# Optimization experiments

Hardware: AMD Instinct MI355X
Metric: run time of the kernel (lower is better)

## Reference

```python
import jax, jax.numpy as jnp
import numpy as np

B, N, D, H, L = 4, 256, 512, 8, 3
HD = D // H
K_SPARSE = max(1, int(N * 0.1))  # top-k edges per node
EPS = 1e-5  # torch LayerNorm default


def _mha(x, Wqkv, bqkv, Wo, bo):
    b, n, d = x.shape
    qkv = x @ Wqkv + bqkv
    q, k, v = jnp.split(qkv, 3, axis=-1)
    rs = lambda t: t.reshape(b, n, H, HD).transpose(0, 2, 1, 3)
    q, k, v = rs(q), rs(k), rs(v)
    att = jax.nn.softmax(jnp.einsum('bhqd,bhkd->bhqk', q, k) * (HD ** -0.5), axis=-1)
    out = jnp.einsum('bhqk,bhkd->bhqd', att, v).transpose(0, 2, 1, 3).reshape(b, n, d)
    return out @ Wo + bo


def _ln(x, g, b):
    m = x.mean(-1, keepdims=True)
    v = ((x - m) ** 2).mean(-1, keepdims=True)
    return (x - m) / jnp.sqrt(v + EPS) * g + b


def setup_inputs() -> dict:
    key = jax.random.key(0)
    ks = iter(jax.random.split(key, 32))
    rn = lambda *s: jax.random.normal(next(ks), s, jnp.float32) * 0.02
    return {
        'x': jax.random.normal(next(ks), (B, N, D), jnp.float32),
        'adjacency': jax.random.uniform(next(ks), (B, N, N), jnp.float32),
        'Wqkv': rn(L, D, 3 * D), 'bqkv': rn(L, 3 * D),
        'Wo': rn(L, D, D), 'bo': rn(L, D),
        'Wp1': rn(L - 1, D, D // 2), 'bp1': rn(L - 1, D // 2),
        'Wp2': rn(L - 1, D // 2, D), 'bp2': rn(L - 1, D),
        'Wfuse': rn(L * D, D), 'bfuse': rn(D),
        'ln_g': jnp.ones((D,), jnp.float32), 'ln_b': jnp.zeros((D,), jnp.float32),
        'We1': rn(2 * D, D), 'be1': rn(D), 'We2': rn(D, 1), 'be2': rn(1),
        'Ws_qkv': rn(D, 3 * D), 'bs_qkv': rn(3 * D),
        'Ws_o': rn(D, D), 'bs_o': rn(D),
    }


def reference(x, adjacency, Wqkv, bqkv, Wo, bo, Wp1, bp1, Wp2, bp2, Wfuse, bfuse,
              ln_g, ln_b, We1, be1, We2, be2, Ws_qkv, bs_qkv, Ws_o, bs_o):
    # --- HierarchicalGraphAttention ---
    cur = x
    level_outs = []
    for l in range(L):  # fixed small hierarchy loop
        a = _mha(cur, Wqkv[l], bqkv[l], Wo[l], bo[l])
        level_outs.append(a)
        if l < L - 1:
            p = jax.nn.relu(a @ Wp1[l] + bp1[l]) @ Wp2[l] + bp2[l]
            cur = p.reshape(B, -1, 2, D).mean(axis=2)  # pairwise pooling halves nodes
    # upsample each level back to N nodes (repeat_interleave), fuse
    fused = [jnp.repeat(o, N // o.shape[1], axis=1) for o in level_outs]
    hier = _ln(jax.nn.relu(jnp.concatenate(fused, axis=-1) @ Wfuse + bfuse), ln_g, ln_b)

    # --- SparseGraphOperations: O(N^2) edge scoring + per-row top-k ---
    # cat([x_i, x_j]) @ We1 == x_i @ We1[:D] + x_j @ We1[D:]
    hi = hier @ We1[:D]                      # [B,N,D]
    hj = hier @ We1[D:] + be1                # [B,N,D]
    pre = hi[:, :, None, :] + hj[:, None, :, :]  # [B,N,N,D]
    scores = jax.nn.sigmoid((jax.nn.relu(pre) @ We2 + be2)[..., 0])  # [B,N,N]
    scores = jnp.where(jnp.eye(N, dtype=bool)[None], 0.0, scores)    # i != j only
    _, idx = jax.lax.top_k(scores, K_SPARSE)  # [B,N,K]
    sparse_adj = jnp.zeros((B, N, N), jnp.float32).at[
        jnp.arange(B)[:, None, None], jnp.arange(N)[None, :, None], idx].set(1.0)

    attended = _mha(hier, Ws_qkv, bs_qkv, Ws_o, bs_o)
    return attended, sparse_adj
```

## Files before the change

### kernel.cpp

```cpp
#include <hip/hip_runtime.h>
#include <math.h>


template <int TM>
__global__ __launch_bounds__(256) void gemm_v6(
    const float* __restrict__ A, const float* __restrict__ W,
    const float* __restrict__ bias, float* __restrict__ C,
    int M, int N, int K, int flags, int wmode,
    const float* __restrict__ W2, const float* __restrict__ bias2)
{
    constexpr int RT = TM / 16;
    __shared__ float As[16][TM + 4];
    __shared__ float Ws[16][68];

    const int tid = threadIdx.x;
    const int tx = tid & 15, ty = tid >> 4;
    const int bm = blockIdx.y * TM, bn = blockIdx.x * 64;

    const float* Wp = W;
    const float* bp = bias;
    int wn = N, wcol = bn;
    if (wmode == 1) {
        int seg = (bm >= 1536) ? 2 : (bm >= 1024) ? 1 : 0;
        Wp += (size_t)seg * 262144;
    } else if (wmode == 3) {
        if (bn < 1536)      { wn = 1536; wcol = bn; }
        else if (bn < 2048) { Wp = W2;           wn = 512; wcol = bn - 1536; bp = nullptr; }
        else                { Wp = W2 + 262144;  wn = 512; wcol = bn - 2048; bp = bias2; }
    }

    constexpr int AV = (TM == 64) ? 4 : 2;
    const int ar = (TM == 64) ? (tid >> 2) : (tid >> 3);
    const int ac = (TM == 64) ? ((tid & 3) << 2) : ((tid & 7) << 1);
    const int wr = tid >> 4;
    const int wc = (tid & 15) << 2;

    const float* Aptr = A + (size_t)(bm + ar) * K + ac;
    const float* Wptr = Wp + (size_t)wr * wn + wcol + wc;

    float acc[RT][4] = {};
    float ra[AV], rw[4];

#define LOADREGS(k0_) do {                                                   \
        const float* ap_ = Aptr + (k0_);                                     \
        if constexpr (TM == 64) {                                            \
            float4 v_ = *(const float4*)ap_;                                 \
            ra[0]=v_.x; ra[1]=v_.y; ra[2]=v_.z; ra[3]=v_.w;                  \
        } else {                                                             \
            float2 v_ = *(const float2*)ap_; ra[0]=v_.x; ra[1]=v_.y;         \
        }                                                                    \
        float4 w_ = *(const float4*)(Wptr + (size_t)(k0_) * wn);             \
        rw[0]=w_.x; rw[1]=w_.y; rw[2]=w_.z; rw[3]=w_.w; } while (0)

    LOADREGS(0);

    for (int k0 = 0; k0 < K; k0 += 16) {
        if (k0) __syncthreads();
        #pragma unroll
        for (int u = 0; u < AV; ++u) As[ac + u][ar] = ra[u];
        #pragma unroll
        for (int u = 0; u < 4; ++u) Ws[wr][wc + u] = rw[u];
        __syncthreads();

        if (k0 + 16 < K) LOADREGS(k0 + 16);

        #pragma unroll
        for (int kk = 0; kk < 16; ++kk) {
            float a[RT];
            if constexpr (RT == 4) {
                float4 t = *(const float4*)&As[kk][ty * 4];
                a[0]=t.x; a[1]=t.y; a[2]=t.z; a[3]=t.w;
            } else {
                float2 t = *(const float2*)&As[kk][ty * 2];
                a[0]=t.x; a[1]=t.y;
            }
            float4 tw = *(const float4*)&Ws[kk][tx * 4];
            float w[4] = {tw.x, tw.y, tw.z, tw.w};
            #pragma unroll
            for (int i = 0; i < RT; ++i)
                #pragma unroll
                for (int j = 0; j < 4; ++j)
                    acc[i][j] = fmaf(a[i], w[j], acc[i][j]);
        }
    }
#undef LOADREGS

    #pragma unroll
    for (int j = 0; j < 4; ++j) {
        const int cn = bn + tx * 4 + j;
        const float bv = bp ? bp[wcol + tx * 4 + j] : 0.f;
        if (flags & 2) {
            #pragma unroll
            for (int pi = 0; pi < RT / 2; ++pi) {
                float f0 = acc[2 * pi][j] + bv;
                float f1 = acc[2 * pi + 1][j] + bv;
                if (flags & 1) { f0 = fmaxf(f0, 0.f); f1 = fmaxf(f1, 0.f); }
                int prow = ((bm + ty * RT) >> 1) + pi;
                C[(size_t)prow * N + cn] = (f0 + f1) * 0.5f;
            }
        } else {
            #pragma unroll
            for (int i = 0; i < RT; ++i) {
                float f = acc[i][j] + bv;
                if (flags & 1) f = fmaxf(f, 0.f);
                C[(size_t)(bm + ty * RT + i) * N + cn] = f;
            }
        }
    }
}

template <int NT>
__global__ __launch_bounds__(256) void attn_v3(
    const float* __restrict__ qkv, float* __restrict__ out, int n, int qstride)
{
    const int lane = threadIdx.x & 63;
    const int w    = threadIdx.x >> 6;
    const int h = blockIdx.y, b = blockIdx.z;
    const int q0 = blockIdx.x * 16;
    const size_t base = (size_t)b * n * qstride;

    __shared__ float q_lds[16][64];
    __shared__ float kv_lds[64][68];
    __shared__ float p_lds[16][256];

    {
        int r = threadIdx.x >> 4, c4 = (threadIdx.x & 15) << 2;
        float4 v = *(const float4*)(qkv + base + (size_t)(q0 + r) * qstride + h * 64 + c4);
        q_lds[r][c4 + 0] = v.x; q_lds[r][c4 + 1] = v.y;
        q_lds[r][c4 + 2] = v.z; q_lds[r][c4 + 3] = v.w;
    }

    const int r0 = w * 4;
    const int sr = threadIdx.x >> 2;
    const int sq = threadIdx.x & 3;

    float s[4][NT];

    #pragma unroll
    for (int t = 0; t < NT; ++t) {
        const int j0 = t * 64;
        __syncthreads();
        {
            const float* src = qkv + base + (size_t)(j0 + sr) * qstride + 512 + h * 64;
            #pragma unroll
            for (int u = 0; u < 4; ++u) {
                int c = u * 4 + sq;
                float4 v = *(const float4*)(src + c * 4);
                *(float4*)&kv_lds[sr][c * 4] = v;
            }
        }
        __syncthreads();
        float c0 = 0.f, c1 = 0.f, c2 = 0.f, c3 = 0.f;
        #pragma unroll
        for (int d = 0; d < 64; d += 4) {
            const float4 kv = *(const float4*)&kv_lds[lane][d];
            const float4 qa = *(const float4*)&q_lds[r0 + 0][d];
            const float4 qb = *(const float4*)&q_lds[r0 + 1][d];
            const float4 qc = *(const float4*)&q_lds[r0 + 2][d];
            const float4 qd = *(const float4*)&q_lds[r0 + 3][d];
            c0 = fmaf(qa.x, kv.x, c0); c0 = fmaf(qa.y, kv.y, c0);
            c0 = fmaf(qa.z, kv.z, c0); c0 = fmaf(qa.w, kv.w, c0);
            c1 = fmaf(qb.x, kv.x, c1); c1 = fmaf(qb.y, kv.y, c1);
            c1 = fmaf(qb.z, kv.z, c1); c1 = fmaf(qb.w, kv.w, c1);
            c2 = fmaf(qc.x, kv.x, c2); c2 = fmaf(qc.y, kv.y, c2);
            c2 = fmaf(qc.z, kv.z, c2); c2 = fmaf(qc.w, kv.w, c2);
            c3 = fmaf(qd.x, kv.x, c3); c3 = fmaf(qd.y, kv.y, c3);
            c3 = fmaf(qd.z, kv.z, c3); c3 = fmaf(qd.w, kv.w, c3);
        }
        s[0][t] = c0 * 0.125f; s[1][t] = c1 * 0.125f;
        s[2][t] = c2 * 0.125f; s[3][t] = c3 * 0.125f;
    }

    double inv[4];
    #pragma unroll
    for (int qr = 0; qr < 4; ++qr) {
        float m = s[qr][0];
        #pragma unroll
        for (int t = 1; t < NT; ++t) m = fmaxf(m, s[qr][t]);
        #pragma unroll
        for (int off = 32; off; off >>= 1) m = fmaxf(m, __shfl_xor(m, off));
        double sum = 0.0;
        #pragma unroll
        for (int t = 0; t < NT; ++t) {
            float p = expf(s[qr][t] - m);
            p_lds[r0 + qr][t * 64 + lane] = p;
            sum += (double)p;
        }
        #pragma unroll
        for (int off = 32; off; off >>= 1) sum += __shfl_xor(sum, off);
        inv[qr] = 1.0 / sum;
    }

    float o0 = 0.f, o1 = 0.f, o2 = 0.f, o3 = 0.f;
    #pragma unroll
    for (int t = 0; t < NT; ++t) {
        const int j0 = t * 64;
        __syncthreads();
        {
            const float* src = qkv + base + (size_t)(j0 + sr) * qstride + 1024 + h * 64;
            #pragma unroll
            for (int u = 0; u < 4; ++u) {
                int c = u * 4 + sq;
                float4 v = *(const float4*)(src + c * 4);
                kv_lds[c * 4 + 0][sr] = v.x;
                kv_lds[c * 4 + 1][sr] = v.y;
                kv_lds[c * 4 + 2][sr] = v.z;
                kv_lds[c * 4 + 3][sr] = v.w;
            }
        }
        __syncthreads();
        #pragma unroll
        for (int jl = 0; jl < 64; jl += 4) {
            const float4 vv = *(const float4*)&kv_lds[lane][jl];
            const float4 pa = *(const float4*)&p_lds[r0 + 0][t * 64 + jl];
            const float4 pb = *(const float4*)&p_lds[r0 + 1][t * 64 + jl];
            const float4 pc = *(const float4*)&p_lds[r0 + 2][t * 64 + jl];
            const float4 pd = *(const float4*)&p_lds[r0 + 3][t * 64 + jl];
            o0 = fmaf(pa.x, vv.x, o0); o0 = fmaf(pa.y, vv.y, o0);
            o0 = fmaf(pa.z, vv.z, o0); o0 = fmaf(pa.w, vv.w, o0);
            o1 = fmaf(pb.x, vv.x, o1); o1 = fmaf(pb.y, vv.y, o1);
            o1 = fmaf(pb.z, vv.z, o1); o1 = fmaf(pb.w, vv.w, o1);
            o2 = fmaf(pc.x, vv.x, o2); o2 = fmaf(pc.y, vv.y, o2);
            o2 = fmaf(pc.z, vv.z, o2); o2 = fmaf(pc.w, vv.w, o2);
            o3 = fmaf(pd.x, vv.x, o3); o3 = fmaf(pd.y, vv.y, o3);
            o3 = fmaf(pd.z, vv.z, o3); o3 = fmaf(pd.w, vv.w, o3);
        }
    }
    const size_t obase = ((size_t)(b * n + q0 + r0)) * 512 + h * 64 + lane;
    out[obase + 0 * 512] = (float)((double)o0 * inv[0]);
    out[obase + 1 * 512] = (float)((double)o1 * inv[1]);
    out[obase + 2 * 512] = (float)((double)o2 * inv[2]);
    out[obase + 3 * 512] = (float)((double)o3 * inv[3]);
}

__global__ __launch_bounds__(64) void ln3_kernel(
    const float* __restrict__ y, const float* __restrict__ bf,
    const float* __restrict__ g, const float* __restrict__ bta,
    float* __restrict__ out)
{
    const int r = blockIdx.x, lane = threadIdx.x;
    const int b = r >> 8, i = r & 255;
    const float* y0 = y + (size_t)r * 512;
    const float* y1 = y + (size_t)(1024 + b * 128 + (i >> 1)) * 512;
    const float* y2 = y + (size_t)(1536 + b * 64 + (i >> 2)) * 512;
    double v[8];
    double sum = 0.0;
    #pragma unroll
    for (int t = 0; t < 8; ++t) {
        int d = t * 64 + lane;
        double s = (double)y0[d] + (double)y1[d] + (double)y2[d] + (double)bf[d];
        s = s > 0.0 ? s : 0.0;
        v[t] = s; sum += s;
    }
    #pragma unroll
    for (int off = 32; off; off >>= 1) sum += __shfl_xor(sum, off);
    const double mean = sum * (1.0 / 512.0);
    double ss = 0.0;
    #pragma unroll
    for (int t = 0; t < 8; ++t) { double d = v[t] - mean; ss += d * d; }
    #pragma unroll
    for (int off = 32; off; off >>= 1) ss += __shfl_xor(ss, off);
    const double rstd = 1.0 / sqrt(ss * (1.0 / 512.0) + 1e-5);
    #pragma unroll
    for (int t = 0; t < 8; ++t) {
        int d = t * 64 + lane;
        out[(size_t)r * 512 + d] =
            (float)((v[t] - mean) * rstd * (double)g[d] + (double)bta[d]);
    }
}

__global__ __launch_bounds__(256) void scores_v4(
    const float* __restrict__ hq, int stride, int off,
    const float* __restrict__ We2, const float* __restrict__ be2,
    float* __restrict__ S)
{
    __shared__ float Hi[128][34];
    __shared__ float Hj[128][34];
    const int b = blockIdx.z;
    const int i0 = blockIdx.y * 32, j0 = blockIdx.x * 32;
    const int tid = threadIdx.x;
    const int tx = tid & 15, ty = tid >> 4;

    const int si = tid >> 3;
    const int sd = (tid & 7) << 2;

    const float* hip = hq + (size_t)(b * 256 + i0 + si) * stride + off + sd;
    const float* hjp = hq + (size_t)(b * 256 + j0 + si) * stride + off + 512 + sd;

    double a00 = 0.0, a01 = 0.0, a10 = 0.0, a11 = 0.0;

    for (int k0 = 0; k0 < 512; k0 += 128) {
        __syncthreads();
        #pragma unroll
        for (int u = 0; u < 4; ++u) {
            const int dch = u * 32 + sd;
            float4 v = *(const float4*)(hip + k0 + u * 32);
            Hi[dch + 0][si] = v.x; Hi[dch + 1][si] = v.y;
            Hi[dch + 2][si] = v.z; Hi[dch + 3][si] = v.w;
            float4 w = *(const float4*)(hjp + k0 + u * 32);
            Hj[dch + 0][si] = w.x; Hj[dch + 1][si] = w.y;
            Hj[dch + 2][si] = w.z; Hj[dch + 3][si] = w.w;
        }
        __syncthreads();
        #pragma unroll 16
        for (int kk = 0; kk < 128; ++kk) {
            const double wv = (double)We2[k0 + kk];
            const float2 hi = *(const float2*)&Hi[kk][ty * 2];
            const float2 hj = *(const float2*)&Hj[kk][tx * 2];
            a00 += (double)fmaxf(hi.x + hj.x, 0.f) * wv;
            a01 += (double)fmaxf(hi.x + hj.y, 0.f) * wv;
            a10 += (double)fmaxf(hi.y + hj.x, 0.f) * wv;
            a11 += (double)fmaxf(hi.y + hj.y, 0.f) * wv;
        }
    }

    const double bb = (double)be2[0];
    const int gi0 = i0 + ty * 2, gj0 = j0 + tx * 2;
    double zz[2][2] = {{a00, a01}, {a10, a11}};
    #pragma unroll
    for (int ii = 0; ii < 2; ++ii)
        #pragma unroll
        for (int jj = 0; jj < 2; ++jj) {
            double z = zz[ii][jj] + bb;
            float sc_ = (float)(1.0 / (1.0 + exp(-z)));
            if (gi0 + ii == gj0 + jj) sc_ = 0.f;
            S[(size_t)(b * 256 + gi0 + ii) * 256 + gj0 + jj] = sc_;
        }
}

__global__ __launch_bounds__(64) void topk_kernel(
    const float* __restrict__ S, float* __restrict__ out)
{
    const int row = blockIdx.x;
    const int lane = threadIdx.x;
    float v[4]; int sel[4] = {0, 0, 0, 0};
    #pragma unroll
    for (int t = 0; t < 4; ++t) v[t] = S[(size_t)row * 256 + t * 64 + lane];
    for (int it = 0; it < 25; ++it) {
        float bv = v[0]; int bi = lane;
        #pragma unroll
        for (int t = 1; t < 4; ++t) {
            int idx = t * 64 + lane;
            if (v[t] > bv) { bv = v[t]; bi = idx; }
        }
        #pragma unroll
        for (int off = 32; off; off >>= 1) {
            float ov = __shfl_xor(bv, off);
            int   oi = __shfl_xor(bi, off);
            if (ov > bv || (ov == bv && oi < bi)) { bv = ov; bi = oi; }
        }
        if ((bi & 63) == lane) { int t = bi >> 6; sel[t] = 1; v[t] = -INFINITY; }
    }
    #pragma unroll
    for (int t = 0; t < 4; ++t)
        out[(size_t)row * 256 + t * 64 + lane] = (float)sel[t];
}

extern "C" void kernel_launch(void* const* d_in, const int* in_sizes, int n_in,
                              void* d_out, int out_size, void* d_ws, size_t ws_size,
                              hipStream_t stream)
{
    const float* x      = (const float*)d_in[0];
    const float* Wqkv   = (const float*)d_in[2];
    const float* bqkv   = (const float*)d_in[3];
    const float* Wo     = (const float*)d_in[4];
    const float* bo     = (const float*)d_in[5];
    const float* Wp1    = (const float*)d_in[6];
    const float* bp1    = (const float*)d_in[7];
    const float* Wp2    = (const float*)d_in[8];
    const float* bp2    = (const float*)d_in[9];
    const float* Wfuse  = (const float*)d_in[10];
    const float* bfuse  = (const float*)d_in[11];
    const float* ln_g   = (const float*)d_in[12];
    const float* ln_b   = (const float*)d_in[13];
    const float* We1    = (const float*)d_in[14];
    const float* be1    = (const float*)d_in[15];
    const float* We2    = (const float*)d_in[16];
    const float* be2    = (const float*)d_in[17];
    const float* Ws_qkv = (const float*)d_in[18];
    const float* bs_qkv = (const float*)d_in[19];
    const float* Ws_o   = (const float*)d_in[20];
    const float* bs_o   = (const float*)d_in[21];

    float* out_att    = (float*)d_out;
    float* out_sparse = out_att + 4 * 256 * 512;

    float* ws    = (float*)d_ws;
    float* qkvb  = ws;
    float* attnb = qkvb + 1572864;
    float* lvls  = attnb + 524288;
    float* poolb = lvls + 917504;
    float* curb  = poolb + 131072;
    float* hier  = curb + 262144;
    float* scb   = hier + 524288;
    float* qh    = scb + 262144;

    float* lvl0 = lvls;
    float* lvl1 = lvls + 1024 * 512;
    float* lvl2 = lvls + 1536 * 512;

    auto G64 = [&](const float* A, const float* W, const float* bias, float* C,
                   int M, int N, int K, int flags, int wmode,
                   const float* W2 = nullptr, const float* bias2 = nullptr) {
        gemm_v6<64><<<dim3(N / 64, M / 64), 256, 0, stream>>>(
            A, W, bias, C, M, N, K, flags, wmode, W2, bias2);
    };
    auto G32 = [&](const float* A, const float* W, const float* bias, float* C,
                   int M, int N, int K, int flags, int wmode) {
        gemm_v6<32><<<dim3(N / 64, M / 32), 256, 0, stream>>>(
            A, W, bias, C, M, N, K, flags, wmode, nullptr, nullptr);
    };

    G64(x, Wqkv, bqkv, qkvb, 1024, 1536, 512, 0, 0);
    attn_v3<4><<<dim3(16, 8, 4), 256, 0, stream>>>(qkvb, attnb, 256, 1536);
    G32(attnb, Wo, bo, lvl0, 1024, 512, 512, 0, 0);
    G32(lvl0, Wp1, bp1, poolb, 1024, 256, 512, 3, 0);
    G32(poolb, Wp2, bp2, curb, 512, 512, 256, 0, 0);

    G64(curb, Wqkv + 512 * 1536, bqkv + 1536, qkvb, 512, 1536, 512, 0, 0);
    attn_v3<2><<<dim3(8, 8, 4), 256, 0, stream>>>(qkvb, attnb, 128, 1536);
    G32(attnb, Wo + 512 * 512, bo + 512, lvl1, 512, 512, 512, 0, 0);
    G32(lvl1, Wp1 + 512 * 256, bp1 + 256, poolb, 512, 256, 512, 3, 0);
    G32(poolb, Wp2 + 256 * 512, bp2 + 512, curb, 256, 512, 256, 0, 0);

    G32(curb, Wqkv + 2 * 512 * 1536, bqkv + 2 * 1536, qkvb, 256, 1536, 512, 0, 0);
    attn_v3<1><<<dim3(4, 8, 4), 256, 0, stream>>>(qkvb, attnb, 64, 1536);
    G32(attnb, Wo + 2 * 512 * 512, bo + 2 * 512, lvl2, 256, 512, 512, 0, 0);

    G64(lvls, Wfuse, nullptr, qkvb, 1792, 512, 512, 0, 1);
    ln3_kernel<<<1024, 64, 0, stream>>>(qkvb, bfuse, ln_g, ln_b, hier);

    G64(hier, Ws_qkv, bs_qkv, qh, 1024, 2560, 512, 0, 3, We1, be1);

    scores_v4<<<dim3(8, 8, 4), 256, 0, stream>>>(qh, 2560, 1536, We2, be2, scb);
    topk_kernel<<<1024, 64, 0, stream>>>(scb, out_sparse);

    attn_v3<4><<<dim3(16, 8, 4), 256, 0, stream>>>(qh, attnb, 256, 2560);
    G32(attnb, Ws_o, bs_o, out_att, 1024, 512, 512, 0, 0);
}
```

Baseline: 391.4 us.

## Use bf16 MFMA GEMMs for final attention projections with transposed weight conversion

Adds a bf16 MFMA GEMM kernel and a weight transpose-and-convert kernel, and runs the final self-attention QKV and output projections on matrix cores. The layernorm and attention kernels also emit bf16 copies of their outputs to feed these GEMMs. The fused QKV+We1 GEMM is split so the edge-score projection stays in fp32 on the old path. This trades extra conversion kernels, extra writes and reduced precision for faster matrix-core math on the final-stage GEMMs.

Result: no change. 383.9 us (-1.9%).

```diff
diff --git a/kernel.cpp b/kernel.cpp
--- a/kernel.cpp
+++ b/kernel.cpp
@@ -1,13 +1,22 @@
 #include <hip/hip_runtime.h>
 #include <math.h>
 
+
+typedef __attribute__((ext_vector_type(8))) short bf16x8;
+typedef __attribute__((ext_vector_type(4))) float f32x4;
+typedef __attribute__((ext_vector_type(8))) unsigned short ushort8v;
+
+__device__ __forceinline__ unsigned short f2bf(float x) {
+    union { float f; unsigned int u; } c; c.f = x;
+    unsigned int r = (c.u + 0x7fffu + ((c.u >> 16) & 1u)) >> 16;
+    return (unsigned short)r;
+}
 
 template <int TM>
 __global__ __launch_bounds__(256) void gemm_v6(
     const float* __restrict__ A, const float* __restrict__ W,
     const float* __restrict__ bias, float* __restrict__ C,
-    int M, int N, int K, int flags, int wmode,
-    const float* __restrict__ W2, const float* __restrict__ bias2)
+    int M, int N, int K, int flags, int wmode)
 {
     constexpr int RT = TM / 16;
     __shared__ float As[16][TM + 4];
@@ -23,10 +32,9 @@
     if (wmode == 1) {
         int seg = (bm >= 1536) ? 2 : (bm >= 1024) ? 1 : 0;
         Wp += (size_t)seg * 262144;
-    } else if (wmode == 3) {
-        if (bn < 1536)      { wn = 1536; wcol = bn; }
-        else if (bn < 2048) { Wp = W2;           wn = 512; wcol = bn - 1536; bp = nullptr; }
-        else                { Wp = W2 + 262144;  wn = 512; wcol = bn - 2048; bp = bias2; }
+    } else if (wmode == 2) {
+        if (bn >= 512) Wp += 262144; else bp = nullptr;
+        wn = 512; wcol = bn & 511;
     }
 
     constexpr int AV = (TM == 64) ? 4 : 2;
@@ -109,9 +117,81 @@
     }
 }
 
+__global__ __launch_bounds__(256) void cvtT_kernel(
+    const float* __restrict__ W, unsigned short* __restrict__ Wt, int K, int N)
+{
+    __shared__ unsigned short t[64][72];
+    const int n0 = blockIdx.x * 64, k0 = blockIdx.y * 64;
+    const int tid = threadIdx.x;
+    const int rr = tid >> 4, c4 = (tid & 15) << 2;
+    #pragma unroll
+    for (int u = 0; u < 4; ++u) {
+        const float4 v = *(const float4*)(W + (size_t)(k0 + rr + u * 16) * N + n0 + c4);
+        t[c4 + 0][rr + u * 16] = f2bf(v.x);
+        t[c4 + 1][rr + u * 16] = f2bf(v.y);
+        t[c4 + 2][rr + u * 16] = f2bf(v.z);
+        t[c4 + 3][rr + u * 16] = f2bf(v.w);
+    }
+    __syncthreads();
+    const int orow = tid >> 2, oc = (tid & 3) << 4;
+    unsigned short* dst = Wt + (size_t)(n0 + orow) * K + k0 + oc;
+    *(ushort8v*)(dst + 0) = *(const ushort8v*)&t[orow][oc + 0];
+    *(ushort8v*)(dst + 8) = *(const ushort8v*)&t[orow][oc + 8];
+}
+
+__global__ __launch_bounds__(256) void mfma_gemm(
+    const unsigned short* __restrict__ Ab, const unsigned short* __restrict__ Bt,
+    const float* __restrict__ bias, float* __restrict__ C,
+    int M, int N, int K, int ldc)
+{
+    const int lane = threadIdx.x & 63;
+    const int wv = threadIdx.x >> 6;
+    const int bn = blockIdx.x * 64;
+    const int bm = blockIdx.y * 128 + wv * 32;
+    const int l15 = lane & 15;
+    const int kb = (lane >> 4) * 8;
+
+    const unsigned short* a0p = Ab + (size_t)(bm + l15) * K + kb;
+    const unsigned short* a1p = a0p + (size_t)16 * K;
+    const unsigned short* bp0 = Bt + (size_t)(bn + l15) * K + kb;
+
+    f32x4 acc[2][4];
+    #pragma unroll
+    for (int i = 0; i < 2; ++i)
+        #pragma unroll
+        for (int j = 0; j < 4; ++j)
+            acc[i][j] = (f32x4){0.f, 0.f, 0.f, 0.f};
+
+    for (int k0 = 0; k0 < K; k0 += 32) {
+        const bf16x8 a0 = *(const bf16x8*)(a0p + k0);
+        const bf16x8 a1 = *(const bf16x8*)(a1p + k0);
+        #pragma unroll
+        for (int nf = 0; nf < 4; ++nf) {
+            const bf16x8 b = *(const bf16x8*)(bp0 + (size_t)nf * 16 * K + k0);
+            acc[0][nf] = __builtin_amdgcn_mfma_f32_16x16x32_bf16(a0, b, acc[0][nf], 0, 0, 0);
+            acc[1][nf] = __builtin_amdgcn_mfma_f32_16x16x32_bf16(a1, b, acc[1][nf], 0, 0, 0);
+        }
+    }
+
+    const int r0 = (lane >> 4) * 4;
+    #pragma unroll
+    for (int mf = 0; mf < 2; ++mf)
+        #pragma unroll
+        for (int nf = 0; nf < 4; ++nf) {
+            const int col = bn + nf * 16 + l15;
+            const float bv = bias ? bias[col] : 0.f;
+            #pragma unroll
+            for (int r = 0; r < 4; ++r) {
+                const int row = bm + mf * 16 + r0 + r;
+                C[(size_t)row * ldc + col] = acc[mf][nf][r] + bv;
+            }
+        }
+}
+
 template <int NT>
 __global__ __launch_bounds__(256) void attn_v3(
-    const float* __restrict__ qkv, float* __restrict__ out, int n, int qstride)
+    const float* __restrict__ qkv, float* __restrict__ out,
+    unsigned short* __restrict__ outb, int n, int qstride)
 {
     const int lane = threadIdx.x & 63;
     const int w    = threadIdx.x >> 6;
@@ -227,16 +307,26 @@
         }
     }
     const size_t obase = ((size_t)(b * n + q0 + r0)) * 512 + h * 64 + lane;
-    out[obase + 0 * 512] = (float)((double)o0 * inv[0]);
-    out[obase + 1 * 512] = (float)((double)o1 * inv[1]);
-    out[obase + 2 * 512] = (float)((double)o2 * inv[2]);
-    out[obase + 3 * 512] = (float)((double)o3 * inv[3]);
+    const float r0v = (float)((double)o0 * inv[0]);
+    const float r1v = (float)((double)o1 * inv[1]);
+    const float r2v = (float)((double)o2 * inv[2]);
+    const float r3v = (float)((double)o3 * inv[3]);
+    out[obase + 0 * 512] = r0v;
+    out[obase + 1 * 512] = r1v;
+    out[obase + 2 * 512] = r2v;
+    out[obase + 3 * 512] = r3v;
+    if (outb) {
+        outb[obase + 0 * 512] = f2bf(r0v);
+        outb[obase + 1 * 512] = f2bf(r1v);
+        outb[obase + 2 * 512] = f2bf(r2v);
+        outb[obase + 3 * 512] = f2bf(r3v);
+    }
 }
 
 __global__ __launch_bounds__(64) void ln3_kernel(
     const float* __restrict__ y, const float* __restrict__ bf,
     const float* __restrict__ g, const float* __restrict__ bta,
-    float* __restrict__ out)
+    float* __restrict__ out, unsigned short* __restrict__ outb)
 {
     const int r = blockIdx.x, lane = threadIdx.x;
     const int b = r >> 8, i = r & 255;
@@ -264,8 +354,9 @@
     #pragma unroll
     for (int t = 0; t < 8; ++t) {
         int d = t * 64 + lane;
-        out[(size_t)r * 512 + d] =
-            (float)((v[t] - mean) * rstd * (double)g[d] + (double)bta[d]);
+        float f = (float)((v[t] - mean) * rstd * (double)g[d] + (double)bta[d]);
+        out[(size_t)r * 512 + d] = f;
+        outb[(size_t)r * 512 + d] = f2bf(f);
     }
 }
 
@@ -393,48 +484,57 @@
     float* curb  = poolb + 131072;
     float* hier  = curb + 262144;
     float* scb   = hier + 524288;
-    float* qh    = scb + 262144;
+    float* hibjb = scb + 262144;
+    float* bfp   = hibjb + 1048576;
+    unsigned short* hier_b  = (unsigned short*)bfp;
+    unsigned short* attnb_b = hier_b + 524288;
+    unsigned short* wqkvT   = attnb_b + 524288;
+    unsigned short* wsoT    = wqkvT + 786432;
 
     float* lvl0 = lvls;
     float* lvl1 = lvls + 1024 * 512;
     float* lvl2 = lvls + 1536 * 512;
 
     auto G64 = [&](const float* A, const float* W, const float* bias, float* C,
-                   int M, int N, int K, int flags, int wmode,
-                   const float* W2 = nullptr, const float* bias2 = nullptr) {
+                   int M, int N, int K, int flags, int wmode) {
         gemm_v6<64><<<dim3(N / 64, M / 64), 256, 0, stream>>>(
-            A, W, bias, C, M, N, K, flags, wmode, W2, bias2);
+            A, W, bias, C, M, N, K, flags, wmode);
     };
     auto G32 = [&](const float* A, const float* W, const float* bias, float* C,
                    int M, int N, int K, int flags, int wmode) {
         gemm_v6<32><<<dim3(N / 64, M / 32), 256, 0, stream>>>(
-            A, W, bias, C, M, N, K, flags, wmode, nullptr, nullptr);
+            A, W, bias, C, M, N, K, flags, wmode);
     };
 
+    cvtT_kernel<<<dim3(1536 / 64, 512 / 64), 256, 0, stream>>>(Ws_qkv, wqkvT, 512, 1536);
+    cvtT_kernel<<<dim3(512 / 64, 512 / 64), 256, 0, stream>>>(Ws_o, wsoT, 512, 512);
+
     G64(x, Wqkv, bqkv, qkvb, 1024, 1536, 512, 0, 0);
-    attn_v3<4><<<dim3(16, 8, 4), 256, 0, stream>>>(qkvb, attnb, 256, 1536);
+    attn_v3<4><<<dim3(16, 8, 4), 256, 0, stream>>>(qkvb, attnb, nullptr, 256, 1536);
     G32(attnb, Wo, bo, lvl0, 1024, 512, 512, 0, 0);
     G32(lvl0, Wp1, bp1, poolb, 1024, 256, 512, 3, 0);
     G32(poolb, Wp2, bp2, curb, 512, 512, 256, 0, 0);
 
     G64(curb, Wqkv + 512 * 1536, bqkv + 1536, qkvb, 512, 1536, 512, 0, 0);
-    attn_v3<2><<<dim3(8, 8, 4), 256, 0, stream>>>(qkvb, attnb, 128, 1536);
+    attn_v3<2><<<dim3(8, 8, 4), 256, 0, stream>>>(qkvb, attnb, nullptr, 128, 1536);
     G32(attnb, Wo + 512 * 512, bo + 512, lvl1, 512, 512, 512, 0, 0);
     G32(lvl1, Wp1 + 512 * 256, bp1 + 256, poolb, 512, 256, 512, 3, 0);
     G32(poolb, Wp2 + 256 * 512, bp2 + 512, curb, 256, 512, 256, 0, 0);
 
     G32(curb, Wqkv + 2 * 512 * 1536, bqkv + 2 * 1536, qkvb, 256, 1536, 512, 0, 0);
-    attn_v3<1><<<dim3(4, 8, 4), 256, 0, stream>>>(qkvb, attnb, 64, 1536);
+    attn_v3<1><<<dim3(4, 8, 4), 256, 0, stream>>>(qkvb, attnb, nullptr, 64, 1536);
     G32(attnb, Wo + 2 * 512 * 512, bo + 2 * 512, lvl2, 256, 512, 512, 0, 0);
 
     G64(lvls, Wfuse, nullptr, qkvb, 1792, 512, 512, 0, 1);
-    ln3_kernel<<<1024, 64, 0, stream>>>(qkvb, bfuse, ln_g, ln_b, hier);
-
-    G64(hier, Ws_qkv, bs_qkv, qh, 1024, 2560, 512, 0, 3, We1, be1);
-
-    scores_v4<<<dim3(8, 8, 4), 256, 0, stream>>>(qh, 2560, 1536, We2, be2, scb);
+    ln3_kernel<<<1024, 64, 0, stream>>>(qkvb, bfuse, ln_g, ln_b, hier, hier_b);
+
+    G64(hier, We1, be1, hibjb, 1024, 1024, 512, 0, 2);
+    scores_v4<<<dim3(8, 8, 4), 256, 0, stream>>>(hibjb, 1024, 0, We2, be2, scb);
     topk_kernel<<<1024, 64, 0, stream>>>(scb, out_sparse);
 
-    attn_v3<4><<<dim3(16, 8, 4), 256, 0, stream>>>(qh, attnb, 256, 2560);
-    G32(attnb, Ws_o, bs_o, out_att, 1024, 512, 512, 0, 0);
-}
+    mfma_gemm<<<dim3(1536 / 64, 1024 / 128), 256, 0, stream>>>(
+        hier_b, wqkvT, bs_qkv, qkvb, 1024, 1536, 512, 1536);
+    attn_v3<4><<<dim3(16, 8, 4), 256, 0, stream>>>(qkvb, attnb, attnb_b, 256, 1536);
+    mfma_gemm<<<dim3(512 / 64, 1024 / 128), 256, 0, stream>>>(
+        attnb_b, wsoT, bs_o, out_att, 1024, 512, 512, 512);
+}
```
